# Kernel tuning notes

Hardware: AMD Instinct MI355X
Metric: run time of the kernel (lower is better)

Reference implementation:

```python
import jax, jax.numpy as jnp
import numpy as np

B, N, D, P = 64, 1024, 256, 256


def setup_inputs() -> dict:
    key = jax.random.key(0)
    kx, k1, k2, k4 = jax.random.split(key, 4)
    x = jax.random.normal(kx, (B, N, D), dtype=jnp.float32)
    # weights ~ random_uniform(-0.05, 0.05) in the original; scale here is irrelevant for math
    w1 = jax.random.uniform(k1, (D, P), dtype=jnp.float32, minval=-0.05, maxval=0.05)
    w2 = jax.random.uniform(k2, (D, P), dtype=jnp.float32, minval=-0.05, maxval=0.05)
    w4 = jax.random.uniform(k4, (P, 1), dtype=jnp.float32, minval=-0.05, maxval=0.05)
    return {"x": x, "w1": w1, "w2": w2, "w4": w4}


def reference(x, w1, w2, w4):
    # x: [B, N, D] (already stacked/transposed; query_n=key_n=values=x in the original)
    q = jax.nn.sigmoid(jnp.einsum('bnd,dp->bnp', x, w1))  # [B,N,P]
    k = jax.nn.sigmoid(jnp.einsum('bnd,dp->bnp', x, w2))  # [B,N,P]
    temper = jnp.sqrt(jnp.asarray(w1.shape[1], x.dtype))
    attn = jax.nn.softmax(jnp.einsum('bnp,bmp->bnm', q, k) / temper, axis=2)  # [B,N,N]
    # dropout(0.1) in the original is inference-identity here
    out = jnp.einsum('bnm,bmd->bnd', attn, x)             # [B,N,D]
    a = jax.nn.softmax(jnp.einsum('bnd,do->bno', out, w4), axis=1)  # [B,N,1]
    sentence = jnp.sum(x * a, axis=1)                     # [B,D]
    return sentence
```

## Files before the change

### kernel.cpp

```cpp
#include <hip/hip_runtime.h>
#include <hip/hip_bf16.h>
#include <cstdint>
#include <cstddef>

constexpr int BB = 64;
constexpr int NN = 1024;
constexpr int DD = 256;
constexpr int PP = 256;

typedef short short8 __attribute__((ext_vector_type(8)));
typedef float f32x4 __attribute__((ext_vector_type(4)));

constexpr float LOG2E = 1.4426950408889634f;

__device__ __forceinline__ unsigned short f2bf(float f) {
    union { __hip_bfloat16 h; unsigned short u; } v;
    v.h = __float2bfloat16(f);
    return v.u;
}

__device__ __forceinline__ float fsigmoid(float x) {
    return __builtin_amdgcn_rcpf(1.f + __builtin_amdgcn_exp2f(x * -LOG2E));
}

__device__ __forceinline__ void async_load16(void* lds, const void* g) {
    __builtin_amdgcn_global_load_lds(
        (const __attribute__((address_space(1))) unsigned int*)g,
        (__attribute__((address_space(3))) unsigned int*)lds, 16, 0, 0);
}

__device__ __forceinline__ void stage32(const unsigned short* base,
                                        unsigned short* lds, int wv, int lane) {
    char* dst0 = (char*)lds + wv * 4096;
    #pragma unroll
    for (int i = 0; i < 4; i++) {
        int row = wv * 8 + i * 2 + (lane >> 5);
        int blk = (lane & 31) ^ (row & 7);
        async_load16(dst0 + i * 1024, (const char*)base + row * 512 + blk * 16);
    }
}

__device__ __forceinline__ short8 lds_frag(const unsigned short* lds, int row, int kidx) {
    uint32_t byte = (uint32_t)(row * 512) + (uint32_t)(((kidx ^ (row & 7)) & 31) << 4);
    return *reinterpret_cast<const short8*>(reinterpret_cast<const char*>(lds) + byte);
}

__global__ void prep_wt(const float* __restrict__ w1, const float* __restrict__ w2,
                        unsigned short* __restrict__ wt) {
    int j = blockIdx.x;
    int d = threadIdx.x;
    const float* w = (j < PP) ? w1 : w2;
    int jj = j & (PP - 1);
    wt[j * DD + d] = f2bf(w[d * PP + jj]);
}

__global__ __launch_bounds__(256, 4) void qk_fused(const float* __restrict__ x,
                                                   const unsigned short* __restrict__ wt,
                                                   const float* __restrict__ w4,
                                                   unsigned short* __restrict__ qb,
                                                   unsigned short* __restrict__ kb,
                                                   float* __restrict__ xv) {
    __shared__ __align__(16) unsigned short wtile[2][8192];
    const int t = threadIdx.x, wv = t >> 6, lane = t & 63, l15 = lane & 15, l4 = lane >> 4;
    const int rowBase = blockIdx.x * 128 + wv * 32;

    stage32(wt, wtile[0], wv, lane);

    short8 xf[2][8];
    float xvp[2] = {0.f, 0.f};
    #pragma unroll
    for (int kc = 0; kc < 8; kc++) {
        float4 w4a = *reinterpret_cast<const float4*>(w4 + kc * 32 + l4 * 8);
        float4 w4b = *reinterpret_cast<const float4*>(w4 + kc * 32 + l4 * 8 + 4);
        #pragma unroll
        for (int s = 0; s < 2; s++) {
            const float* xr = x + (size_t)(rowBase + s * 16 + l15) * DD + kc * 32 + l4 * 8;
            float4 a = *reinterpret_cast<const float4*>(xr);
            float4 b = *reinterpret_cast<const float4*>(xr + 4);
            xvp[s] += a.x * w4a.x + a.y * w4a.y + a.z * w4a.z + a.w * w4a.w
                    + b.x * w4b.x + b.y * w4b.y + b.z * w4b.z + b.w * w4b.w;
            short8 f;
            f[0] = (short)f2bf(a.x); f[1] = (short)f2bf(a.y);
            f[2] = (short)f2bf(a.z); f[3] = (short)f2bf(a.w);
            f[4] = (short)f2bf(b.x); f[5] = (short)f2bf(b.y);
            f[6] = (short)f2bf(b.z); f[7] = (short)f2bf(b.w);
            xf[s][kc] = f;
        }
    }
    #pragma unroll
    for (int s = 0; s < 2; s++) {
        xvp[s] += __shfl_xor(xvp[s], 16);
        xvp[s] += __shfl_xor(xvp[s], 32);
        if (l4 == 0) xv[rowBase + s * 16 + l15] = xvp[s];
    }

    __syncthreads();
    int buf = 0;
    for (int ct = 0; ct < 16; ct++) {
        if (ct + 1 < 16) stage32(wt + (size_t)(ct + 1) * 32 * DD, wtile[buf ^ 1], wv, lane);
        unsigned short* outp = (ct < 8) ? qb : kb;
        const int pc0 = (ct & 7) * 32;
        #pragma unroll
        for (int st = 0; st < 2; st++) {
            f32x4 acc0 = {0.f, 0.f, 0.f, 0.f};
            f32x4 acc1 = {0.f, 0.f, 0.f, 0.f};
            #pragma unroll
            for (int kc = 0; kc < 8; kc++) {
                short8 wf = lds_frag(wtile[buf], st * 16 + l15, kc * 4 + l4);
                acc0 = __builtin_amdgcn_mfma_f32_16x16x32_bf16(wf, xf[0][kc], acc0, 0, 0, 0);
                acc1 = __builtin_amdgcn_mfma_f32_16x16x32_bf16(wf, xf[1][kc], acc1, 0, 0, 0);
            }
            const int pc = pc0 + st * 16 + l4 * 4;
            ushort4 pk;
            pk.x = f2bf(fsigmoid(acc0[0]));
            pk.y = f2bf(fsigmoid(acc0[1]));
            pk.z = f2bf(fsigmoid(acc0[2]));
            pk.w = f2bf(fsigmoid(acc0[3]));
            *reinterpret_cast<ushort4*>(outp + (size_t)(rowBase + l15) * PP + pc) = pk;
            pk.x = f2bf(fsigmoid(acc1[0]));
            pk.y = f2bf(fsigmoid(acc1[1]));
            pk.z = f2bf(fsigmoid(acc1[2]));
            pk.w = f2bf(fsigmoid(acc1[3]));
            *reinterpret_cast<ushort4*>(outp + (size_t)(rowBase + 16 + l15) * PP + pc) = pk;
        }
        __syncthreads();
        buf ^= 1;
    }
}

__global__ __launch_bounds__(512, 2) void attn_logit(const unsigned short* __restrict__ qb,
                                                     const unsigned short* __restrict__ kb,
                                                     const float* __restrict__ xv,
                                                     float* __restrict__ numo,
                                                     float* __restrict__ deno) {
    __shared__ __align__(16) unsigned short kq[256 * 256];
    __shared__ float xvs[256];
    const int t = threadIdx.x, wv = t >> 6, lane = t & 63, l15 = lane & 15, l4 = lane >> 4;
    const int wg = blockIdx.x;
    const int xcd = wg & 7, r_ = wg >> 3;
    const int quarter = r_ & 3;
    const int b = xcd + 8 * (r_ >> 2);
    const unsigned short* kbb = kb + ((size_t)b * NN + quarter * 256) * PP;

    {
        char* dst0 = (char*)kq + wv * 16384;
        #pragma unroll
        for (int i = 0; i < 16; i++) {
            int row = wv * 32 + i * 2 + (lane >> 5);
            int blk = (lane & 31) ^ (row & 7);
            async_load16(dst0 + i * 1024, (const char*)kbb + row * 512 + blk * 16);
        }
    }
    if (t < 256) xvs[t] = xv[b * NN + quarter * 256 + t];
    __syncthreads();

    #pragma unroll 1
    for (int p = 0; p < 2; p++) {
        short8 qf[4][8];
        const int q0 = b * NN + p * 512 + wv * 64;
        #pragma unroll
        for (int s = 0; s < 4; s++) {
            const unsigned short* qrow = qb + (size_t)(q0 + s * 16 + l15) * PP;
            #pragma unroll
            for (int kc = 0; kc < 8; kc++)
                qf[s][kc] = *reinterpret_cast<const short8*>(qrow + kc * 32 + l4 * 8);
        }
        float den[4][4], num[4][4];
        #pragma unroll
        for (int s = 0; s < 4; s++)
            #pragma unroll
            for (int r = 0; r < 4; r++) { den[s][r] = 0.f; num[s][r] = 0.f; }

        #pragma unroll 4
        for (int mc = 0; mc < 16; mc++) {
            f32x4 z = {0.f, 0.f, 0.f, 0.f};
            f32x4 a[4] = {z, z, z, z};
            #pragma unroll
            for (int kc = 0; kc < 8; kc++) {
                short8 kf = lds_frag(kq, mc * 16 + l15, kc * 4 + l4);
                a[0] = __builtin_amdgcn_mfma_f32_16x16x32_bf16(qf[0][kc], kf, a[0], 0, 0, 0);
                a[1] = __builtin_amdgcn_mfma_f32_16x16x32_bf16(qf[1][kc], kf, a[1], 0, 0, 0);
                a[2] = __builtin_amdgcn_mfma_f32_16x16x32_bf16(qf[2][kc], kf, a[2], 0, 0, 0);
                a[3] = __builtin_amdgcn_mfma_f32_16x16x32_bf16(qf[3][kc], kf, a[3], 0, 0, 0);
            }
            float xvv = xvs[mc * 16 + l15];
            #pragma unroll
            for (int s = 0; s < 4; s++)
                #pragma unroll
                for (int r = 0; r < 4; r++) {
                    float e = __builtin_amdgcn_exp2f(a[s][r] * (0.0625f * LOG2E));
                    den[s][r] += e;
                    num[s][r] += e * xvv;
                }
        }
        #pragma unroll
        for (int s = 0; s < 4; s++)
            #pragma unroll
            for (int r = 0; r < 4; r++) {
                #pragma unroll
                for (int off = 1; off < 16; off <<= 1) {
                    den[s][r] += __shfl_xor(den[s][r], off);
                    num[s][r] += __shfl_xor(num[s][r], off);
                }
            }
        if (l15 == 0) {
            #pragma unroll
            for (int s = 0; s < 4; s++)
                #pragma unroll
                for (int r = 0; r < 4; r++) {
                    int n = p * 512 + wv * 64 + s * 16 + l4 * 4 + r;
                    size_t o = (size_t)quarter * BB * NN + (size_t)b * NN + n;
                    numo[o] = num[s][r];
                    deno[o] = den[s][r];
                }
        }
    }
}

__global__ __launch_bounds__(256) void sent_partial(const float* __restrict__ x,
                                                    const float* __restrict__ numo,
                                                    const float* __restrict__ deno,
                                                    float* __restrict__ part) {
    __shared__ float al[64];
    __shared__ float redA[4];
    __shared__ float redB[4];
    const int b = blockIdx.x, ch = blockIdx.y;
    const int t = threadIdx.x;
    float l[4];
    #pragma unroll
    for (int i = 0; i < 4; i++) {
        int n = b * NN + t + i * 256;
        float ns = 0.f, ds = 0.f;
        #pragma unroll
        for (int q = 0; q < 4; q++) {
            ns += numo[(size_t)q * BB * NN + n];
            ds += deno[(size_t)q * BB * NN + n];
        }
        l[i] = ns / ds;
    }
    float mx = fmaxf(fmaxf(l[0], l[1]), fmaxf(l[2], l[3]));
    #pragma unroll
    for (int off = 1; off < 64; off <<= 1) mx = fmaxf(mx, __shfl_xor(mx, off));
    if ((t & 63) == 0) redA[t >> 6] = mx;
    __syncthreads();
    mx = fmaxf(fmaxf(redA[0], redA[1]), fmaxf(redA[2], redA[3]));
    float e[4], es = 0.f;
    #pragma unroll
    for (int i = 0; i < 4; i++) { e[i] = __expf(l[i] - mx); es += e[i]; }
    #pragma unroll
    for (int off = 1; off < 64; off <<= 1) es += __shfl_xor(es, off);
    if ((t & 63) == 0) redB[t >> 6] = es;
    __syncthreads();
    float inv = 1.f / (redB[0] + redB[1] + redB[2] + redB[3]);
    int ei = ch >> 2;
    float sel = (ei == 0) ? e[0] : (ei == 1) ? e[1] : (ei == 2) ? e[2] : e[3];
    if ((t >> 6) == (ch & 3)) al[t & 63] = sel * inv;
    __syncthreads();
    float acc = 0.f;
    const float* xb = x + ((size_t)b * NN + ch * 64) * DD + t;
    #pragma unroll 8
    for (int n = 0; n < 64; n++)
        acc += al[n] * xb[(size_t)n * DD];
    part[(b * 16 + ch) * DD + t] = acc;
}

__global__ void sent_final(const float* __restrict__ part, float* __restrict__ out) {
    int b = blockIdx.x, t = threadIdx.x;
    float s = 0.f;
    #pragma unroll
    for (int c = 0; c < 16; c++) s += part[(b * 16 + c) * DD + t];
    out[b * DD + t] = s;
}

extern "C" void kernel_launch(void* const* d_in, const int* in_sizes, int n_in,
                              void* d_out, int out_size, void* d_ws, size_t ws_size,
                              hipStream_t stream) {
    (void)in_sizes; (void)n_in; (void)out_size; (void)ws_size;
    const float* x  = (const float*)d_in[0];
    const float* w1 = (const float*)d_in[1];
    const float* w2 = (const float*)d_in[2];
    const float* w4 = (const float*)d_in[3];
    float* out = (float*)d_out;

    char* ws = (char*)d_ws;
    const size_t MB = 1024 * 1024;
    unsigned short* qb   = (unsigned short*)(ws);
    unsigned short* kb   = (unsigned short*)(ws + 32 * MB);
    unsigned short* wt   = (unsigned short*)(ws + 64 * MB);
    float*          xv   = (float*)(ws + 64 * MB + 256 * 1024);
    float*          num  = (float*)(ws + 64 * MB + 512 * 1024);
    float*          den  = (float*)(ws + 64 * MB + 1536 * 1024);
    float*          part = (float*)(ws);

    prep_wt<<<dim3(2 * PP), dim3(DD), 0, stream>>>(w1, w2, wt);
    qk_fused<<<dim3(BB * NN / 128), dim3(256), 0, stream>>>(x, wt, w4, qb, kb, xv);
    attn_logit<<<dim3(4 * BB), dim3(512), 0, stream>>>(qb, kb, xv, num, den);
    sent_partial<<<dim3(BB, 16), dim3(256), 0, stream>>>(x, num, den, part);
    sent_final<<<dim3(BB), dim3(DD), 0, stream>>>(part, out);
}
```

Before: 117.1 us.

## Stage full 128KB weight half in LDS per 512-thread block in qk_fused

```diff
diff --git a/kernel.cpp b/kernel.cpp
--- a/kernel.cpp
+++ b/kernel.cpp
@@ -29,12 +29,12 @@
         (__attribute__((address_space(3))) unsigned int*)lds, 16, 0, 0);
 }
 
-__device__ __forceinline__ void stage32(const unsigned short* base,
-                                        unsigned short* lds, int wv, int lane) {
-    char* dst0 = (char*)lds + wv * 4096;
-    #pragma unroll
-    for (int i = 0; i < 4; i++) {
-        int row = wv * 8 + i * 2 + (lane >> 5);
+__device__ __forceinline__ void stage256(const unsigned short* base,
+                                         unsigned short* lds, int wv, int lane) {
+    char* dst0 = (char*)lds + wv * 16384;
+    #pragma unroll
+    for (int i = 0; i < 16; i++) {
+        int row = wv * 32 + i * 2 + (lane >> 5);
         int blk = (lane & 31) ^ (row & 7);
         async_load16(dst0 + i * 1024, (const char*)base + row * 512 + blk * 16);
     }
@@ -54,17 +54,17 @@
     wt[j * DD + d] = f2bf(w[d * PP + jj]);
 }
 
-__global__ __launch_bounds__(256, 4) void qk_fused(const float* __restrict__ x,
+__global__ __launch_bounds__(512, 2) void qk_fused(const float* __restrict__ x,
                                                    const unsigned short* __restrict__ wt,
                                                    const float* __restrict__ w4,
                                                    unsigned short* __restrict__ qb,
                                                    unsigned short* __restrict__ kb,
                                                    float* __restrict__ xv) {
-    __shared__ __align__(16) unsigned short wtile[2][8192];
+    __shared__ __align__(16) unsigned short wl[256 * 256];
     const int t = threadIdx.x, wv = t >> 6, lane = t & 63, l15 = lane & 15, l4 = lane >> 4;
-    const int rowBase = blockIdx.x * 128 + wv * 32;
-
-    stage32(wt, wtile[0], wv, lane);
+    const int rowBase = blockIdx.x * 256 + wv * 32;
+
+    stage256(wt, wl, wv, lane);
 
     short8 xf[2][8];
     float xvp[2] = {0.f, 0.f};
@@ -95,22 +95,26 @@
     }
 
     __syncthreads();
-    int buf = 0;
-    for (int ct = 0; ct < 16; ct++) {
-        if (ct + 1 < 16) stage32(wt + (size_t)(ct + 1) * 32 * DD, wtile[buf ^ 1], wv, lane);
-        unsigned short* outp = (ct < 8) ? qb : kb;
-        const int pc0 = (ct & 7) * 32;
-        #pragma unroll
-        for (int st = 0; st < 2; st++) {
+
+    #pragma unroll 1
+    for (int h = 0; h < 2; h++) {
+        if (h == 1) {
+            __syncthreads();
+            stage256(wt + 256 * DD, wl, wv, lane);
+            __syncthreads();
+        }
+        unsigned short* outp = h ? kb : qb;
+        #pragma unroll 1
+        for (int pt = 0; pt < 16; pt++) {
             f32x4 acc0 = {0.f, 0.f, 0.f, 0.f};
             f32x4 acc1 = {0.f, 0.f, 0.f, 0.f};
             #pragma unroll
             for (int kc = 0; kc < 8; kc++) {
-                short8 wf = lds_frag(wtile[buf], st * 16 + l15, kc * 4 + l4);
+                short8 wf = lds_frag(wl, pt * 16 + l15, kc * 4 + l4);
                 acc0 = __builtin_amdgcn_mfma_f32_16x16x32_bf16(wf, xf[0][kc], acc0, 0, 0, 0);
                 acc1 = __builtin_amdgcn_mfma_f32_16x16x32_bf16(wf, xf[1][kc], acc1, 0, 0, 0);
             }
-            const int pc = pc0 + st * 16 + l4 * 4;
+            const int pc = pt * 16 + l4 * 4;
             ushort4 pk;
             pk.x = f2bf(fsigmoid(acc0[0]));
             pk.y = f2bf(fsigmoid(acc0[1]));
@@ -123,8 +127,6 @@
             pk.w = f2bf(fsigmoid(acc1[3]));
             *reinterpret_cast<ushort4*>(outp + (size_t)(rowBase + 16 + l15) * PP + pc) = pk;
         }
-        __syncthreads();
-        buf ^= 1;
     }
 }
 
@@ -142,15 +144,7 @@
     const int b = xcd + 8 * (r_ >> 2);
     const unsigned short* kbb = kb + ((size_t)b * NN + quarter * 256) * PP;
 
-    {
-        char* dst0 = (char*)kq + wv * 16384;
-        #pragma unroll
-        for (int i = 0; i < 16; i++) {
-            int row = wv * 32 + i * 2 + (lane >> 5);
-            int blk = (lane & 31) ^ (row & 7);
-            async_load16(dst0 + i * 1024, (const char*)kbb + row * 512 + blk * 16);
-        }
-    }
+    stage256(kbb, kq, wv, lane);
     if (t < 256) xvs[t] = xv[b * NN + quarter * 256 + t];
     __syncthreads();
 
@@ -293,7 +287,7 @@
     float*          part = (float*)(ws);
 
     prep_wt<<<dim3(2 * PP), dim3(DD), 0, stream>>>(w1, w2, wt);
-    qk_fused<<<dim3(BB * NN / 128), dim3(256), 0, stream>>>(x, wt, w4, qb, kb, xv);
+    qk_fused<<<dim3(BB * NN / 256), dim3(512), 0, stream>>>(x, wt, w4, qb, kb, xv);
     attn_logit<<<dim3(4 * BB), dim3(512), 0, stream>>>(qb, kb, xv, num, den);
     sent_partial<<<dim3(BB, 16), dim3(256), 0, stream>>>(x, num, den, part);
     sent_final<<<dim3(BB), dim3(DD), 0, stream>>>(part, out);
```

Result: faster. 96.21 us (-17.8%).
